# Optimization experiments

Measured on AMD Instinct MI355X. Metric: run time of the kernel, lower is better.

## Reference

```python
import jax, jax.numpy as jnp
import numpy as np

SEQ_LEN = 720
PRED_LEN = 720
CHANNEL_DIM = 321
BATCH = 64


def setup_inputs() -> dict:
    key = jax.random.key(0)
    kx, kw, kb = jax.random.split(key, 3)
    x = jax.random.normal(kx, (BATCH, SEQ_LEN, CHANNEL_DIM), dtype=jnp.float32)
    # per-channel Linear(seq_len, pred_len): weight [C, pred_len, seq_len], bias [C, pred_len]
    bound = 1.0 / np.sqrt(SEQ_LEN)
    W = jax.random.uniform(kw, (CHANNEL_DIM, PRED_LEN, SEQ_LEN), minval=-bound, maxval=bound, dtype=jnp.float32)
    b = jax.random.uniform(kb, (CHANNEL_DIM, PRED_LEN), minval=-bound, maxval=bound, dtype=jnp.float32)
    return {"x": x, "W": W, "b": b}


def reference(x, W, b):
    # x: [B, S, C]; per-channel linear along the time axis.
    # torch: x.transpose(1,2) -> [B, C, S]; y[:, i] = Linear_i(x[:, i]); transpose back.
    # Batched grouped GEMM over channels in one einsum.
    y = jnp.einsum('bsc,cps->bcp', x, W) + b  # [B, C, P]
    return y.transpose(0, 2, 1)  # [B, P, C]
```

## Files before the change

### kernel.cpp

```cpp
#include <hip/hip_runtime.h>
#include <hip/hip_bf16.h>


#define SEQ   720
#define PRED  720
#define CH    321
#define BATCH 64
#define RTOT  (BATCH*SEQ)
#define BN1   48
#define NT1   15
#define BN    144
#define NCHUNK 21
#define NGROUP (NCHUNK*5)

typedef __attribute__((ext_vector_type(8))) short short8;
typedef __attribute__((ext_vector_type(4))) float f32x4;
typedef __attribute__((ext_vector_type(4))) unsigned short us4;
typedef unsigned int u32;

__device__ __forceinline__ short bf16bits(float f) {
    return __builtin_bit_cast(short, __float2bfloat16(f));
}

__device__ __forceinline__ void gload16(const void* g, void* l) {
    __builtin_amdgcn_global_load_lds((const __attribute__((address_space(1))) u32*)g,
                                     (__attribute__((address_space(3))) u32*)l, 16, 0, 0);
}

__global__ __launch_bounds__(256) void xpose_kernel(const float* __restrict__ x,
                                                    unsigned short* __restrict__ xt) {
    __shared__ float tile[64][33];
    const int bid = blockIdx.x;
    const int rt = bid % (RTOT/64);
    const int ct = bid / (RTOT/64);
    const int r0 = rt*64, c0 = ct*32;
    const int t  = threadIdx.x;
    const int cl = t & 31, rl0 = t >> 5;
    const int cg = c0 + cl;
    if (cg < CH) {
#pragma unroll
        for (int j = 0; j < 8; ++j) {
            int rl = rl0 + j*8;
            tile[rl][cl] = x[(size_t)(r0+rl)*CH + cg];
        }
    }
    __syncthreads();
#pragma unroll
    for (int j = 0; j < 8; ++j) {
        int idx = t + j*256;
        int c_l = idx >> 6;
        int r_l = idx & 63;
        if (c0 + c_l < CH)
            xt[(size_t)(c0+c_l)*RTOT + r0 + r_l] = (unsigned short)bf16bits(tile[r_l][c_l]);
    }
}

template<bool STAGED>
__global__ __launch_bounds__(64) void gemm1w_kernel(
        const float* __restrict__ W, const float* __restrict__ bias,
        const unsigned short* __restrict__ xt, void* __restrict__ outp) {
    __shared__ __align__(16) float          Bl[2][BN1*64];
    __shared__ __align__(16) unsigned short Al[2][64*64];

    const int bid = blockIdx.x;
    const int c   = bid / NT1;
    const int pt  = bid % NT1;
    const int p0  = pt * BN1;
    const int lane = threadIdx.x & 63;
    const int row = lane & 15, kch = lane >> 4;

    const float* Wc          = W  + (size_t)c * ((size_t)PRED * SEQ);
    const unsigned short* Xc = xt + (size_t)c * RTOT;

    auto stage = [&](int buf, int kk) {
        const bool tail = (kk == 11);
#pragma unroll
        for (int i = 0; i < 12; ++i) {
            const int r = 4*i + (lane >> 4);
            int sc = (lane & 15) ^ (r & 15);
            if (tail) sc &= 3;
            gload16(Wc + (size_t)(p0 + r)*SEQ + kk*64 + sc*4, &Bl[buf][i*256]);
        }
#pragma unroll
        for (int i = 0; i < 8; ++i) {
            const int r = 8*i + (lane >> 3);
            int sc = (lane & 7) ^ (r & 7);
            if (tail) sc &= 1;
            gload16(Xc + (size_t)r*SEQ + kk*64 + sc*8, &Al[buf][i*512]);
        }
    };

    f32x4 acc[4][3] = {};

    auto compute = [&](int buf, int s, bool ztail) {
        short8 Af[4];
#pragma unroll
        for (int mi = 0; mi < 4; ++mi) {
            const int r2 = mi*16 + row;
            const int qa = (s*4 + kch) ^ (r2 & 7);
            Af[mi] = *reinterpret_cast<const short8*>(&Al[buf][r2*64 + qa*8]);
        }
        short8 Bf[3];
#pragma unroll
        for (int ni = 0; ni < 3; ++ni) {
            const int r2  = ni*16 + row;
            const int qlo = (s*8 + 2*kch)     ^ (r2 & 15);
            const int qhi = (s*8 + 2*kch + 1) ^ (r2 & 15);
            f32x4 lo = *reinterpret_cast<const f32x4*>(&Bl[buf][r2*64 + qlo*4]);
            f32x4 hi = *reinterpret_cast<const f32x4*>(&Bl[buf][r2*64 + qhi*4]);
            short8 v;
#pragma unroll
            for (int j = 0; j < 4; ++j) { v[j] = bf16bits(lo[j]); v[4+j] = bf16bits(hi[j]); }
            Bf[ni] = v;
        }
        if (ztail && kch >= 2) {
            short8 z = {};
            Bf[0] = z; Bf[1] = z; Bf[2] = z;
        }
#pragma unroll
        for (int mi = 0; mi < 4; ++mi)
#pragma unroll
            for (int ni = 0; ni < 3; ++ni)
                acc[mi][ni] = __builtin_amdgcn_mfma_f32_16x16x32_bf16(
                                  Af[mi], Bf[ni], acc[mi][ni], 0, 0, 0);
    };

    stage(0, 0);
    stage(1, 1);
    for (int k = 0; k < 11; ++k) {
        const int buf = k & 1;
        asm volatile("s_waitcnt vmcnt(20)" ::: "memory");
        __builtin_amdgcn_sched_barrier(0);
        compute(buf, 0, false);
        compute(buf, 1, false);
        asm volatile("s_waitcnt lgkmcnt(0)" ::: "memory");
        __builtin_amdgcn_sched_barrier(0);
        if (k <= 9) stage(buf, k + 2);
    }
    {
        asm volatile("s_waitcnt vmcnt(0)" ::: "memory");
        __builtin_amdgcn_sched_barrier(0);
        compute(1, 0, true);
    }

    const int col   = lane & 15;
    const int rquad = lane >> 4;
    if (STAGED) {
        unsigned short* stg = (unsigned short*)outp;
#pragma unroll
        for (int ni = 0; ni < 3; ++ni) {
            const int p = p0 + ni*16 + col;
            const float bv = bias[(size_t)c*PRED + p];
#pragma unroll
            for (int mi = 0; mi < 4; ++mi) {
                us4 u;
#pragma unroll
                for (int r = 0; r < 4; ++r)
                    u[r] = (unsigned short)bf16bits(acc[mi][ni][r] + bv);
                *reinterpret_cast<us4*>(
                    stg + ((size_t)c*PRED + p)*BATCH + mi*16 + rquad*4) = u;
            }
        }
    } else {
        float* outf = (float*)outp;
#pragma unroll
        for (int ni = 0; ni < 3; ++ni) {
            const int p = p0 + ni*16 + col;
            const float bv = bias[(size_t)c*PRED + p];
#pragma unroll
            for (int mi = 0; mi < 4; ++mi)
#pragma unroll
                for (int r = 0; r < 4; ++r) {
                    const int b = mi*16 + rquad*4 + r;
                    outf[((size_t)b*PRED + p)*CH + c] = acc[mi][ni][r] + bv;
                }
        }
    }
}

__global__ __launch_bounds__(192) void gemm_fallback_kernel(
        const float* __restrict__ W, const float* __restrict__ bias,
        const float* __restrict__ x, float* __restrict__ outp) {
    const int bid  = blockIdx.x;
    const int g    = (bid & 7) + 8*((bid >> 3) >> 4);
    const int coff = (bid >> 3) & 15;
    if (g >= NGROUP) return;
    const int c  = (g % NCHUNK)*16 + coff;
    if (c >= CH) return;
    const int p0 = (g / NCHUNK) * BN;
    const int tid = threadIdx.x, wv = tid >> 6, lane = tid & 63;
    const int row = lane & 15, kch = lane >> 4, nb = p0 + wv*48;
    const float* Wc = W + (size_t)c * ((size_t)PRED * SEQ);
    f32x4 acc[4][3] = {};
    for (int k = 0; k < 23; ++k) {
        const int kc = (k == 22) ? (kch & 1) : kch;
        const int s  = k*32 + kc*8;
        short8 Af[4], Bf[3];
#pragma unroll
        for (int mi = 0; mi < 4; ++mi) {
            short8 v;
#pragma unroll
            for (int j = 0; j < 8; ++j)
                v[j] = bf16bits(x[((size_t)(mi*16 + row)*SEQ + s + j)*CH + c]);
            Af[mi] = v;
        }
#pragma unroll
        for (int ni = 0; ni < 3; ++ni) {
            const float* p = Wc + (size_t)(nb + ni*16 + row)*SEQ + s;
            short8 v;
#pragma unroll
            for (int j = 0; j < 4; ++j) { v[j] = bf16bits(p[j]); v[4+j] = bf16bits(p[4+j]); }
            Bf[ni] = v;
        }
        if (k == 22 && kch >= 2) { short8 z = {}; Bf[0] = z; Bf[1] = z; Bf[2] = z; }
#pragma unroll
        for (int mi = 0; mi < 4; ++mi)
#pragma unroll
            for (int ni = 0; ni < 3; ++ni)
                acc[mi][ni] = __builtin_amdgcn_mfma_f32_16x16x32_bf16(
                                  Af[mi], Bf[ni], acc[mi][ni], 0, 0, 0);
    }
    const int col = lane & 15, rquad = lane >> 4;
#pragma unroll
    for (int ni = 0; ni < 3; ++ni) {
        const int p = nb + ni*16 + col;
        const float bv = bias[(size_t)c*PRED + p];
#pragma unroll
        for (int mi = 0; mi < 4; ++mi)
#pragma unroll
            for (int r = 0; r < 4; ++r)
                outp[((size_t)(mi*16 + rquad*4 + r)*PRED + p)*CH + c] = acc[mi][ni][r] + bv;
    }
}

__global__ __launch_bounds__(256) void unstage_kernel(const unsigned short* __restrict__ stage,
                                                      float* __restrict__ out) {
    const int p  = blockIdx.x;
    const int c0 = blockIdx.y * 128;
    const int cn = (CH - c0 < 128) ? (CH - c0) : 128;
    __shared__ float tl[128][65];
    const int t = threadIdx.x;
    {
        const int b   = t & 63;
        const int ci0 = t >> 6;
        for (int ci = ci0; ci < cn; ci += 4) {
            unsigned short us = stage[((size_t)(c0+ci)*PRED + p)*BATCH + b];
            tl[ci][b] = __builtin_bit_cast(float, (u32)us << 16);
        }
    }
    __syncthreads();
    {
        const int cl = t & 127;
        const int b0 = t >> 7;
        if (cl < cn)
#pragma unroll
            for (int bb = b0; bb < BATCH; bb += 2)
                out[((size_t)bb*PRED + p)*CH + c0 + cl] = tl[cl][bb];
    }
}

extern "C" void kernel_launch(void* const* d_in, const int* in_sizes, int n_in,
                              void* d_out, int out_size, void* d_ws, size_t ws_size,
                              hipStream_t stream) {
    const float* x    = (const float*)d_in[0];
    const float* W    = (const float*)d_in[1];
    const float* bias = (const float*)d_in[2];
    float* out        = (float*)d_out;

    const size_t xt_bytes    = (size_t)CH * RTOT * sizeof(unsigned short);
    const size_t stage_bytes = (size_t)CH * PRED * BATCH * sizeof(unsigned short);

    if (ws_size >= xt_bytes + stage_bytes) {
        unsigned short* xtp = (unsigned short*)d_ws;
        unsigned short* stg = (unsigned short*)((char*)d_ws + xt_bytes);
        xpose_kernel<<<dim3((RTOT/64) * 11), dim3(256), 0, stream>>>(x, xtp);
        gemm1w_kernel<true><<<dim3(CH * NT1), dim3(64), 0, stream>>>(W, bias, xtp, stg);
        unstage_kernel<<<dim3(PRED, 3), dim3(256), 0, stream>>>(stg, out);
    } else if (ws_size >= xt_bytes) {
        unsigned short* xtp = (unsigned short*)d_ws;
        xpose_kernel<<<dim3((RTOT/64) * 11), dim3(256), 0, stream>>>(x, xtp);
        gemm1w_kernel<false><<<dim3(CH * NT1), dim3(64), 0, stream>>>(W, bias, xtp, out);
    } else {
        gemm_fallback_kernel<<<dim3(8 * 14 * 16), dim3(192), 0, stream>>>(
            W, bias, x, out);
    }
}
```

Before: 217.7 us.

## Shrink GEMM tile to 16 outputs and stage full W rows into LDS upfront

Each block now computes 16 prediction rows instead of 48. The entire 16x720 fp32 weight slab is loaded into LDS once at the start, and only the transposed-x tiles are double-buffered along K. This triples the grid size, raising parallelism and making W loading a single bulk transfer. In exchange, each wave does a third of the MFMA work per x tile load, so x tiles are re-read three times as often. LDS per block also grows to about 64KB, which may limit occupancy.

```diff
diff --git a/kernel.cpp b/kernel.cpp
--- a/kernel.cpp
+++ b/kernel.cpp
@@ -7,8 +7,8 @@
 #define CH    321
 #define BATCH 64
 #define RTOT  (BATCH*SEQ)
-#define BN1   48
-#define NT1   15
+#define BNL   16
+#define NTL   45
 #define BN    144
 #define NCHUNK 21
 #define NGROUP (NCHUNK*5)
@@ -56,43 +56,46 @@
 }
 
 template<bool STAGED>
-__global__ __launch_bounds__(64) void gemm1w_kernel(
+__global__ __launch_bounds__(64) void gemm_lin_kernel(
         const float* __restrict__ W, const float* __restrict__ bias,
         const unsigned short* __restrict__ xt, void* __restrict__ outp) {
-    __shared__ __align__(16) float          Bl[2][BN1*64];
+    __shared__ __align__(16) float          Bl[BNL*768];
     __shared__ __align__(16) unsigned short Al[2][64*64];
 
     const int bid = blockIdx.x;
-    const int c   = bid / NT1;
-    const int pt  = bid % NT1;
-    const int p0  = pt * BN1;
+    const int c   = bid / NTL;
+    const int pt  = bid % NTL;
+    const int p0  = pt * BNL;
     const int lane = threadIdx.x & 63;
     const int row = lane & 15, kch = lane >> 4;
 
     const float* Wc          = W  + (size_t)c * ((size_t)PRED * SEQ);
     const unsigned short* Xc = xt + (size_t)c * RTOT;
 
-    auto stage = [&](int buf, int kk) {
-        const bool tail = (kk == 11);
-#pragma unroll
-        for (int i = 0; i < 12; ++i) {
-            const int r = 4*i + (lane >> 4);
-            int sc = (lane & 15) ^ (r & 15);
-            if (tail) sc &= 3;
-            gload16(Wc + (size_t)(p0 + r)*SEQ + kk*64 + sc*4, &Bl[buf][i*256]);
-        }
+    auto stageB = [&]() {
+#pragma unroll
+        for (int r = 0; r < 16; ++r)
+#pragma unroll
+            for (int j = 0; j < 3; ++j) {
+                const int a = 4*j + (lane >> 4);
+                int lc = (a << 4) | ((lane & 15) ^ r);
+                if (lc > 179) lc = 176;
+                gload16(Wc + (size_t)(p0 + r)*SEQ + lc*4, &Bl[(r*192 + j*64)*4]);
+            }
+    };
+    auto stageA = [&](int buf, int kk) {
 #pragma unroll
         for (int i = 0; i < 8; ++i) {
             const int r = 8*i + (lane >> 3);
             int sc = (lane & 7) ^ (r & 7);
-            if (tail) sc &= 1;
+            if (kk == 11) sc &= 1;
             gload16(Xc + (size_t)r*SEQ + kk*64 + sc*8, &Al[buf][i*512]);
         }
     };
 
-    f32x4 acc[4][3] = {};
-
-    auto compute = [&](int buf, int s, bool ztail) {
+    f32x4 acc[4] = {};
+
+    auto compute = [&](int buf, int k, int s, bool ztail) {
         short8 Af[4];
 #pragma unroll
         for (int mi = 0; mi < 4; ++mi) {
@@ -100,81 +103,71 @@
             const int qa = (s*4 + kch) ^ (r2 & 7);
             Af[mi] = *reinterpret_cast<const short8*>(&Al[buf][r2*64 + qa*8]);
         }
-        short8 Bf[3];
-#pragma unroll
-        for (int ni = 0; ni < 3; ++ni) {
-            const int r2  = ni*16 + row;
-            const int qlo = (s*8 + 2*kch)     ^ (r2 & 15);
-            const int qhi = (s*8 + 2*kch + 1) ^ (r2 & 15);
-            f32x4 lo = *reinterpret_cast<const f32x4*>(&Bl[buf][r2*64 + qlo*4]);
-            f32x4 hi = *reinterpret_cast<const f32x4*>(&Bl[buf][r2*64 + qhi*4]);
+        short8 Bf;
+        {
+            const int lc0 = k*16 + s*8 + 2*kch;
+            const int ph0 = (lc0 & ~15) | ((lc0 & 15) ^ row);
+            const int ph1 = ((lc0+1) & ~15) | (((lc0+1) & 15) ^ row);
+            f32x4 lo = *reinterpret_cast<const f32x4*>(&Bl[row*768 + ph0*4]);
+            f32x4 hi = *reinterpret_cast<const f32x4*>(&Bl[row*768 + ph1*4]);
             short8 v;
 #pragma unroll
             for (int j = 0; j < 4; ++j) { v[j] = bf16bits(lo[j]); v[4+j] = bf16bits(hi[j]); }
-            Bf[ni] = v;
-        }
-        if (ztail && kch >= 2) {
-            short8 z = {};
-            Bf[0] = z; Bf[1] = z; Bf[2] = z;
-        }
-#pragma unroll
-        for (int mi = 0; mi < 4; ++mi)
-#pragma unroll
-            for (int ni = 0; ni < 3; ++ni)
-                acc[mi][ni] = __builtin_amdgcn_mfma_f32_16x16x32_bf16(
-                                  Af[mi], Bf[ni], acc[mi][ni], 0, 0, 0);
+            Bf = v;
+        }
+        if (ztail && kch >= 2) { short8 z = {}; Bf = z; }
+#pragma unroll
+        for (int mi = 0; mi < 4; ++mi)
+            acc[mi] = __builtin_amdgcn_mfma_f32_16x16x32_bf16(Af[mi], Bf, acc[mi], 0, 0, 0);
     };
 
-    stage(0, 0);
-    stage(1, 1);
+    stageB();
+    stageA(0, 0);
+    asm volatile("s_waitcnt vmcnt(0)" ::: "memory");
+    __builtin_amdgcn_sched_barrier(0);
+    stageA(1, 1);
     for (int k = 0; k < 11; ++k) {
         const int buf = k & 1;
-        asm volatile("s_waitcnt vmcnt(20)" ::: "memory");
-        __builtin_amdgcn_sched_barrier(0);
-        compute(buf, 0, false);
-        compute(buf, 1, false);
+        if (k > 0) {
+            asm volatile("s_waitcnt vmcnt(8)" ::: "memory");
+            __builtin_amdgcn_sched_barrier(0);
+        }
+        compute(buf, k, 0, false);
+        compute(buf, k, 1, false);
         asm volatile("s_waitcnt lgkmcnt(0)" ::: "memory");
         __builtin_amdgcn_sched_barrier(0);
-        if (k <= 9) stage(buf, k + 2);
+        if (k <= 9) stageA(buf, k + 2);
     }
     {
         asm volatile("s_waitcnt vmcnt(0)" ::: "memory");
         __builtin_amdgcn_sched_barrier(0);
-        compute(1, 0, true);
+        compute(1, 11, 0, true);
     }
 
     const int col   = lane & 15;
     const int rquad = lane >> 4;
+    const int p     = p0 + col;
+    const float bv  = bias[(size_t)c*PRED + p];
     if (STAGED) {
         unsigned short* stg = (unsigned short*)outp;
 #pragma unroll
-        for (int ni = 0; ni < 3; ++ni) {
-            const int p = p0 + ni*16 + col;
-            const float bv = bias[(size_t)c*PRED + p];
-#pragma unroll
-            for (int mi = 0; mi < 4; ++mi) {
-                us4 u;
-#pragma unroll
-                for (int r = 0; r < 4; ++r)
-                    u[r] = (unsigned short)bf16bits(acc[mi][ni][r] + bv);
-                *reinterpret_cast<us4*>(
-                    stg + ((size_t)c*PRED + p)*BATCH + mi*16 + rquad*4) = u;
-            }
+        for (int mi = 0; mi < 4; ++mi) {
+            us4 u;
+#pragma unroll
+            for (int r = 0; r < 4; ++r)
+                u[r] = (unsigned short)bf16bits(acc[mi][r] + bv);
+            *reinterpret_cast<us4*>(
+                stg + ((size_t)c*PRED + p)*BATCH + mi*16 + rquad*4) = u;
         }
     } else {
         float* outf = (float*)outp;
 #pragma unroll
-        for (int ni = 0; ni < 3; ++ni) {
-            const int p = p0 + ni*16 + col;
-            const float bv = bias[(size_t)c*PRED + p];
-#pragma unroll
-            for (int mi = 0; mi < 4; ++mi)
-#pragma unroll
-                for (int r = 0; r < 4; ++r) {
-                    const int b = mi*16 + rquad*4 + r;
-                    outf[((size_t)b*PRED + p)*CH + c] = acc[mi][ni][r] + bv;
-                }
-        }
+        for (int mi = 0; mi < 4; ++mi)
+#pragma unroll
+            for (int r = 0; r < 4; ++r) {
+                const int b = mi*16 + rquad*4 + r;
+                outf[((size_t)b*PRED + p)*CH + c] = acc[mi][r] + bv;
+            }
     }
 }
 
@@ -274,12 +267,12 @@
         unsigned short* xtp = (unsigned short*)d_ws;
         unsigned short* stg = (unsigned short*)((char*)d_ws + xt_bytes);
         xpose_kernel<<<dim3((RTOT/64) * 11), dim3(256), 0, stream>>>(x, xtp);
-        gemm1w_kernel<true><<<dim3(CH * NT1), dim3(64), 0, stream>>>(W, bias, xtp, stg);
+        gemm_lin_kernel<true><<<dim3(CH * NTL), dim3(64), 0, stream>>>(W, bias, xtp, stg);
         unstage_kernel<<<dim3(PRED, 3), dim3(256), 0, stream>>>(stg, out);
     } else if (ws_size >= xt_bytes) {
         unsigned short* xtp = (unsigned short*)d_ws;
         xpose_kernel<<<dim3((RTOT/64) * 11), dim3(256), 0, stream>>>(x, xtp);
-        gemm1w_kernel<false><<<dim3(CH * NT1), dim3(64), 0, stream>>>(W, bias, xtp, out);
+        gemm_lin_kernel<false><<<dim3(CH * NTL), dim3(64), 0, stream>>>(W, bias, xtp, out);
     } else {
         gemm_fallback_kernel<<<dim3(8 * 14 * 16), dim3(192), 0, stream>>>(
             W, bias, x, out);
```

New measurement: 298.2 us. 37.0% more time.

## Load W tiles directly into registers and remap blocks to group channels

Applied to the files above, without the earlier changes.

The GEMM kernel stops staging the fp32 weight tile through LDS. Each lane now issues global_load_dwordx4 straight into registers, and the k-step is halved to 32 with two register buffers so the loads overlap compute. Only the bf16 x tile still goes through a smaller LDS double buffer. Block indices are remapped so eight adjacent channels share a p-tile group, and launch bounds request 3 waves per SIMD. This cuts LDS traffic and footprint and removes an LDS round trip for W, at the cost of more registers, hand-written vmcnt accounting, and less coalesced per-lane W reads.

```diff
diff --git a/kernel.cpp b/kernel.cpp
--- a/kernel.cpp
+++ b/kernel.cpp
@@ -9,6 +9,8 @@
 #define RTOT  (BATCH*SEQ)
 #define BN1   48
 #define NT1   15
+#define CPG   120
+#define NBLKG 41
 #define BN    144
 #define NCHUNK 21
 #define NGROUP (NCHUNK*5)
@@ -56,15 +58,15 @@
 }
 
 template<bool STAGED>
-__global__ __launch_bounds__(64) void gemm1w_kernel(
+__global__ __launch_bounds__(64, 3) void gemm_reg_kernel(
         const float* __restrict__ W, const float* __restrict__ bias,
         const unsigned short* __restrict__ xt, void* __restrict__ outp) {
-    __shared__ __align__(16) float          Bl[2][BN1*64];
-    __shared__ __align__(16) unsigned short Al[2][64*64];
+    __shared__ __align__(16) unsigned short Al[2][64*32];
 
     const int bid = blockIdx.x;
-    const int c   = bid / NT1;
-    const int pt  = bid % NT1;
+    const int c   = (bid / CPG) * 8 + (bid & 7);
+    const int pt  = (bid % CPG) >> 3;
+    if (c >= CH) return;
     const int p0  = pt * BN1;
     const int lane = threadIdx.x & 63;
     const int row = lane & 15, kch = lane >> 4;
@@ -72,51 +74,68 @@
     const float* Wc          = W  + (size_t)c * ((size_t)PRED * SEQ);
     const unsigned short* Xc = xt + (size_t)c * RTOT;
 
-    auto stage = [&](int buf, int kk) {
-        const bool tail = (kk == 11);
-#pragma unroll
-        for (int i = 0; i < 12; ++i) {
-            const int r = 4*i + (lane >> 4);
-            int sc = (lane & 15) ^ (r & 15);
-            if (tail) sc &= 3;
-            gload16(Wc + (size_t)(p0 + r)*SEQ + kk*64 + sc*4, &Bl[buf][i*256]);
-        }
-#pragma unroll
-        for (int i = 0; i < 8; ++i) {
-            const int r = 8*i + (lane >> 3);
-            int sc = (lane & 7) ^ (r & 7);
-            if (tail) sc &= 1;
-            gload16(Xc + (size_t)r*SEQ + kk*64 + sc*8, &Al[buf][i*512]);
+    u32 vb[3], vbt[3];
+#pragma unroll
+    for (int ni = 0; ni < 3; ++ni) {
+        vb[ni]  = (u32)(((p0 + ni*16 + row) * SEQ) * 4 + kch*32);
+        vbt[ni] = (u32)(((p0 + ni*16 + row) * SEQ) * 4 + (kch & 1)*32);
+    }
+
+    auto stageA = [&](int buf, int kk) {
+#pragma unroll
+        for (int i = 0; i < 4; ++i) {
+            const int r  = i*16 + (lane >> 2);
+            int sc = (lane & 3) ^ (r & 3);
+            if (kk == 22) sc &= 1;
+            gload16(Xc + (size_t)r*SEQ + kk*32 + sc*8, &Al[buf][i*512]);
         }
     };
+#define LOADB(B, KK, TAILC)                                                     \
+    {                                                                           \
+        _Pragma("unroll")                                                       \
+        for (int ni = 0; ni < 3; ++ni) {                                        \
+            u32 off = ((TAILC) ? vbt[ni] : vb[ni]) + (u32)(KK)*128u;            \
+            asm volatile("global_load_dwordx4 %0, %1, %2"                       \
+                         : "=&v"(B[2*ni])                                       \
+                         : "v"(off), "s"(Wc) : "memory");                       \
+            asm volatile("global_load_dwordx4 %0, %1, %2 offset:16"             \
+                         : "=&v"(B[2*ni+1])                                     \
+                         : "v"(off), "s"(Wc) : "memory");                       \
+        }                                                                       \
+    }
+#define WAITB(B, N)                                                             \
+    asm volatile("s_waitcnt vmcnt(" #N ")"                                      \
+                 : "+v"(B[0]), "+v"(B[1]), "+v"(B[2]),                          \
+                   "+v"(B[3]), "+v"(B[4]), "+v"(B[5])                           \
+                 :: "memory");                                                  \
+    __builtin_amdgcn_sched_barrier(0);
+#define LGKM0                                                                   \
+    asm volatile("s_waitcnt lgkmcnt(0)" ::: "memory");                          \
+    __builtin_amdgcn_sched_barrier(0);
 
     f32x4 acc[4][3] = {};
-
-    auto compute = [&](int buf, int s, bool ztail) {
+    f32x4 B0[6], B1[6];
+
+    auto compute = [&](const unsigned short* Ab, f32x4 (&B)[6], bool ztail) {
         short8 Af[4];
 #pragma unroll
         for (int mi = 0; mi < 4; ++mi) {
             const int r2 = mi*16 + row;
-            const int qa = (s*4 + kch) ^ (r2 & 7);
-            Af[mi] = *reinterpret_cast<const short8*>(&Al[buf][r2*64 + qa*8]);
+            const int qa = kch ^ (r2 & 3);
+            Af[mi] = *reinterpret_cast<const short8*>(&Ab[r2*32 + qa*8]);
         }
         short8 Bf[3];
 #pragma unroll
         for (int ni = 0; ni < 3; ++ni) {
-            const int r2  = ni*16 + row;
-            const int qlo = (s*8 + 2*kch)     ^ (r2 & 15);
-            const int qhi = (s*8 + 2*kch + 1) ^ (r2 & 15);
-            f32x4 lo = *reinterpret_cast<const f32x4*>(&Bl[buf][r2*64 + qlo*4]);
-            f32x4 hi = *reinterpret_cast<const f32x4*>(&Bl[buf][r2*64 + qhi*4]);
             short8 v;
 #pragma unroll
-            for (int j = 0; j < 4; ++j) { v[j] = bf16bits(lo[j]); v[4+j] = bf16bits(hi[j]); }
+            for (int j = 0; j < 4; ++j) {
+                v[j]   = bf16bits(B[2*ni][j]);
+                v[4+j] = bf16bits(B[2*ni+1][j]);
+            }
             Bf[ni] = v;
         }
-        if (ztail && kch >= 2) {
-            short8 z = {};
-            Bf[0] = z; Bf[1] = z; Bf[2] = z;
-        }
+        if (ztail && kch >= 2) { short8 z = {}; Bf[0] = z; Bf[1] = z; Bf[2] = z; }
 #pragma unroll
         for (int mi = 0; mi < 4; ++mi)
 #pragma unroll
@@ -125,22 +144,26 @@
                                   Af[mi], Bf[ni], acc[mi][ni], 0, 0, 0);
     };
 
-    stage(0, 0);
-    stage(1, 1);
-    for (int k = 0; k < 11; ++k) {
-        const int buf = k & 1;
-        asm volatile("s_waitcnt vmcnt(20)" ::: "memory");
+    stageA(0, 0); LOADB(B0, 0, false);
+    stageA(1, 1); LOADB(B1, 1, false);
+
+    for (int kk = 0; kk < 22; kk += 2) {
+        WAITB(B0, 10);
+        compute(&Al[0][0], B0, false);
+        LGKM0;
+        if (kk < 20) { stageA(0, kk + 2); LOADB(B0, kk + 2, false); }
+        else         { stageA(0, 22);     LOADB(B0, 22,     true ); }
         __builtin_amdgcn_sched_barrier(0);
-        compute(buf, 0, false);
-        compute(buf, 1, false);
-        asm volatile("s_waitcnt lgkmcnt(0)" ::: "memory");
+
+        WAITB(B1, 10);
+        compute(&Al[1][0], B1, false);
+        LGKM0;
+        if (kk < 20) { stageA(1, kk + 3); LOADB(B1, kk + 3, false); }
         __builtin_amdgcn_sched_barrier(0);
-        if (k <= 9) stage(buf, k + 2);
     }
     {
-        asm volatile("s_waitcnt vmcnt(0)" ::: "memory");
-        __builtin_amdgcn_sched_barrier(0);
-        compute(1, 0, true);
+        WAITB(B0, 0);
+        compute(&Al[0][0], B0, true);
     }
 
     const int col   = lane & 15;
@@ -176,6 +199,9 @@
                 }
         }
     }
+#undef LOADB
+#undef WAITB
+#undef LGKM0
 }
 
 __global__ __launch_bounds__(192) void gemm_fallback_kernel(
@@ -274,12 +300,12 @@
         unsigned short* xtp = (unsigned short*)d_ws;
         unsigned short* stg = (unsigned short*)((char*)d_ws + xt_bytes);
         xpose_kernel<<<dim3((RTOT/64) * 11), dim3(256), 0, stream>>>(x, xtp);
-        gemm1w_kernel<true><<<dim3(CH * NT1), dim3(64), 0, stream>>>(W, bias, xtp, stg);
+        gemm_reg_kernel<true><<<dim3(NBLKG * CPG), dim3(64), 0, stream>>>(W, bias, xtp, stg);
         unstage_kernel<<<dim3(PRED, 3), dim3(256), 0, stream>>>(stg, out);
     } else if (ws_size >= xt_bytes) {
         unsigned short* xtp = (unsigned short*)d_ws;
         xpose_kernel<<<dim3((RTOT/64) * 11), dim3(256), 0, stream>>>(x, xtp);
-        gemm1w_kernel<false><<<dim3(CH * NT1), dim3(64), 0, stream>>>(W, bias, xtp, out);
+        gemm_reg_kernel<false><<<dim3(NBLKG * CPG), dim3(64), 0, stream>>>(W, bias, xtp, out);
     } else {
         gemm_fallback_kernel<<<dim3(8 * 14 * 16), dim3(192), 0, stream>>>(
             W, bias, x, out);
```

After: 242.9 us. 11.6% more time.
